# Kernel tuning notes

Measured on AMD Instinct MI355X. Metric: run time of the kernel, lower is better.

## Reference

```python
import jax, jax.numpy as jnp
import numpy as np

B, D, W = 65536, 256, 1024

def setup_inputs() -> dict:
    key = jax.random.key(0)
    k1, k2, k3, k4 = jax.random.split(key, 4)
    z = jax.random.normal(k1, (B, D), dtype=jnp.float32)
    # PyTorch Linear init: U(-1/sqrt(fan_in), 1/sqrt(fan_in))
    s1 = 1.0 / np.sqrt(D)
    s2 = 1.0 / np.sqrt(W)
    W1 = jax.random.uniform(k2, (W, D), dtype=jnp.float32, minval=-s1, maxval=s1)
    b1 = jax.random.uniform(k3, (W,), dtype=jnp.float32, minval=-s1, maxval=s1)
    W2 = jax.random.uniform(k4, (D, W), dtype=jnp.float32, minval=-s2, maxval=s2)
    t = jnp.zeros((1,), dtype=jnp.float32)
    return {"t": t, "z": z, "W1": W1, "b1": b1, "W2": W2}

def reference(t, z, W1, b1, W2):
    # dynamics: f(z) = W2 @ softplus(W1 z + b1)   (t is unused; autonomous ODE)
    pre = z @ W1.T + b1                 # [B, W]
    h = jax.nn.softplus(pre)            # [B, W]
    dz_dt = h @ W2.T                    # [B, D]
    # trace of Jacobian, analytic:
    # df_i/dz_i = sum_j W2[i,j] * sigmoid(pre_j) * W1[j,i]
    # => trace_b = sigmoid(pre_b) . M, with M_j = sum_i W1[j,i] * W2[i,j]
    M = jnp.einsum('ji,ij->j', W1, W2)  # [W]
    trace = jax.nn.sigmoid(pre) @ M     # [B]
    dlogpz_dt = -trace[:, None]         # [B, 1]
    return (dz_dt, dlogpz_dt)
```

## Files before the change

### kernel.cpp

```cpp
#include <hip/hip_runtime.h>
#include <cstdint>
#include <cstddef>

#define B_N 65536
#define D_N 256
#define W_N 1024

typedef __bf16 bf16x8 __attribute__((ext_vector_type(8)));
typedef float f32x4 __attribute__((ext_vector_type(4)));
typedef unsigned short u16x8 __attribute__((ext_vector_type(8)));

__device__ __forceinline__ unsigned short f2bf(float f) {
  unsigned u = __float_as_uint(f);
  u += 0x7fffu + ((u >> 16) & 1u);
  return (unsigned short)(u >> 16);
}

__global__ __launch_bounds__(256) void prep_kernel(
    const float* __restrict__ W1, const float* __restrict__ W2,
    unsigned short* __restrict__ W1b, unsigned short* __restrict__ W2b,
    float* __restrict__ M) {
  const int j = blockIdx.x;
  const int t = threadIdx.x;
  const int gid = j * 256 + t;
  float w1 = W1[gid];
  float w2g = W2[gid];
  W1b[gid] = f2bf(w1);
  W2b[gid] = f2bf(w2g);
  float p = w1 * W2[t * W_N + j];
  #pragma unroll
  for (int m = 32; m; m >>= 1) p += __shfl_xor(p, m);
  __shared__ float red[4];
  if ((t & 63) == 0) red[t >> 6] = p;
  __syncthreads();
  if (t == 0) M[j] = red[0] + red[1] + red[2] + red[3];
}

__global__ __launch_bounds__(256, 2) void flow_kernel(
    const float* __restrict__ z, const float* __restrict__ b1,
    const unsigned short* __restrict__ W1b, const unsigned short* __restrict__ W2b,
    const float* __restrict__ M, float* __restrict__ dz, float* __restrict__ tr) {
  __shared__ __align__(16) unsigned short z_sh[64 * 256];
  __shared__ __align__(16) unsigned short h_sh[64 * 256];

  const int tid = threadIdx.x;
  const int wave = tid >> 6;
  const int lane = tid & 63;
  const int l15 = lane & 15;
  const int q = lane >> 4;
  const int row0 = blockIdx.x * 64;

  #pragma unroll
  for (int it = 0; it < 8; ++it) {
    int id = it * 256 + tid;
    int m = id >> 5;
    int o = id & 31;
    const float* gp = z + (size_t)(row0 + m) * D_N + o * 8;
    f32x4 a = *(const f32x4*)gp;
    f32x4 b = *(const f32x4*)(gp + 4);
    u16x8 v;
    v[0] = f2bf(a[0]); v[1] = f2bf(a[1]); v[2] = f2bf(a[2]); v[3] = f2bf(a[3]);
    v[4] = f2bf(b[0]); v[5] = f2bf(b[1]); v[6] = f2bf(b[2]); v[7] = f2bf(b[3]);
    int slot = (((o >> 2) * 4 + (m >> 4)) * 64 + (o & 3) * 16 + (m & 15));
    *(u16x8*)(z_sh + slot * 8) = v;
  }
  __syncthreads();

  f32x4 acc2[4][4];
  #pragma unroll
  for (int a = 0; a < 4; ++a)
    #pragma unroll
    for (int b = 0; b < 4; ++b)
      acc2[a][b] = (f32x4){0.f, 0.f, 0.f, 0.f};
  float trp[4][4];
  #pragma unroll
  for (int a = 0; a < 4; ++a)
    #pragma unroll
    for (int r = 0; r < 4; ++r) trp[a][r] = 0.f;

  #pragma unroll 1
  for (int c = 0; c < 4; ++c) {
    const int j0 = c * 256;

    f32x4 acc1[4][4];
    #pragma unroll
    for (int a = 0; a < 4; ++a)
      #pragma unroll
      for (int b = 0; b < 4; ++b)
        acc1[a][b] = (f32x4){0.f, 0.f, 0.f, 0.f};

    #pragma unroll
    for (int ks = 0; ks < 8; ++ks) {
      bf16x8 afr[4];
      #pragma unroll
      for (int tm = 0; tm < 4; ++tm)
        afr[tm] = *(const bf16x8*)(z_sh + ((ks * 4 + tm) * 64 + lane) * 8);
      bf16x8 bfr[4];
      #pragma unroll
      for (int tn = 0; tn < 4; ++tn)
        bfr[tn] = *(const bf16x8*)(W1b +
            (size_t)(j0 + wave * 64 + tn * 16 + l15) * D_N + ks * 32 + q * 8);
      #pragma unroll
      for (int tm = 0; tm < 4; ++tm)
        #pragma unroll
        for (int tn = 0; tn < 4; ++tn)
          acc1[tm][tn] = __builtin_amdgcn_mfma_f32_16x16x32_bf16(
              afr[tm], bfr[tn], acc1[tm][tn], 0, 0, 0);
    }

    __syncthreads();

    #pragma unroll
    for (int tn = 0; tn < 4; ++tn) {
      const int jl = wave * 64 + tn * 16 + l15;
      const int jg = j0 + jl;
      const float b1v = b1[jg];
      const float Mv = M[jg];
      const int slot_base = ((jl >> 5) * 4) * 64 + ((jl >> 3) & 3) * 16;
      const int byte_lo = (jl & 7);
      #pragma unroll
      for (int tm = 0; tm < 4; ++tm) {
        #pragma unroll
        for (int r = 0; r < 4; ++r) {
          float x = acc1[tm][tn][r] + b1v;
          float e = __expf(-fabsf(x));
          float inv = __builtin_amdgcn_rcpf(1.0f + e);
          float sig = (x >= 0.f) ? inv : (1.0f - inv);
          float sp = fmaxf(x, 0.f) + __logf(1.0f + e);
          trp[tm][r] += sig * Mv;
          int slot = slot_base + tm * 64 + (q * 4 + r);
          h_sh[slot * 8 + byte_lo] = f2bf(sp);
        }
      }
    }
    __syncthreads();

    #pragma unroll
    for (int ks = 0; ks < 8; ++ks) {
      bf16x8 afr[4];
      #pragma unroll
      for (int tm = 0; tm < 4; ++tm)
        afr[tm] = *(const bf16x8*)(h_sh + ((ks * 4 + tm) * 64 + lane) * 8);
      bf16x8 bfr[4];
      #pragma unroll
      for (int tn = 0; tn < 4; ++tn)
        bfr[tn] = *(const bf16x8*)(W2b +
            (size_t)(wave * 64 + tn * 16 + l15) * W_N + j0 + ks * 32 + q * 8);
      #pragma unroll
      for (int tm = 0; tm < 4; ++tm)
        #pragma unroll
        for (int tn = 0; tn < 4; ++tn)
          acc2[tm][tn] = __builtin_amdgcn_mfma_f32_16x16x32_bf16(
              afr[tm], bfr[tn], acc2[tm][tn], 0, 0, 0);
    }
  }

  #pragma unroll
  for (int tm = 0; tm < 4; ++tm)
    #pragma unroll
    for (int tn = 0; tn < 4; ++tn)
      #pragma unroll
      for (int r = 0; r < 4; ++r)
        dz[(size_t)(row0 + tm * 16 + q * 4 + r) * D_N + wave * 64 + tn * 16 + l15] =
            acc2[tm][tn][r];

  #pragma unroll
  for (int tm = 0; tm < 4; ++tm) {
    #pragma unroll
    for (int r = 0; r < 4; ++r) {
      float v = trp[tm][r];
      v += __shfl_xor(v, 1);
      v += __shfl_xor(v, 2);
      v += __shfl_xor(v, 4);
      v += __shfl_xor(v, 8);
      if (l15 == 0) atomicAdd(tr + row0 + tm * 16 + q * 4 + r, -v);
    }
  }
}

extern "C" void kernel_launch(void* const* d_in, const int* in_sizes, int n_in,
                              void* d_out, int out_size, void* d_ws, size_t ws_size,
                              hipStream_t stream) {
  (void)in_sizes; (void)n_in; (void)out_size; (void)ws_size;
  const float* z  = (const float*)d_in[1];
  const float* W1 = (const float*)d_in[2];
  const float* b1 = (const float*)d_in[3];
  const float* W2 = (const float*)d_in[4];
  float* dz = (float*)d_out;
  float* tr = dz + (size_t)B_N * D_N;

  unsigned short* W1b = (unsigned short*)d_ws;
  unsigned short* W2b = W1b + (size_t)W_N * D_N;
  float* M = (float*)(W2b + (size_t)W_N * D_N);

  hipMemsetAsync(tr, 0, B_N * sizeof(float), stream);
  prep_kernel<<<dim3(W_N), dim3(256), 0, stream>>>(W1, W2, W1b, W2b, M);
  flow_kernel<<<dim3(B_N / 64), dim3(256), 0, stream>>>(z, b1, W1b, W2b, M, dz, tr);
}
```

Before: 261.5 us.

## Software-pipeline GEMM1 of next chunk with softplus epilogue of current chunk

Restructures the chunk loop so the first GEMM for the next 256-column chunk runs interleaved with the transcendental epilogue (softplus/sigmoid) of the current chunk. Two accumulator sets are used, which lets MFMA work overlap with VALU exp/log work. The second GEMM also runs at raised wave priority via s_setprio. The cost is more live registers (two 4x4 f32x4 accumulator sets plus acc2), which risks spilling or lower occupancy under launch_bounds(256,2).

```diff
diff --git a/kernel.cpp b/kernel.cpp
--- a/kernel.cpp
+++ b/kernel.cpp
@@ -78,81 +78,113 @@
     #pragma unroll
     for (int r = 0; r < 4; ++r) trp[a][r] = 0.f;
 
+  f32x4 accA[4][4], accB[4][4];
+
+#define ZERO_ACC(A_)                                                          \
+  _Pragma("unroll") for (int za_ = 0; za_ < 4; ++za_)                         \
+  _Pragma("unroll") for (int zb_ = 0; zb_ < 4; ++zb_)                         \
+    A_[za_][zb_] = (f32x4){0.f, 0.f, 0.f, 0.f};
+
+#define G1_STEP(J0_, ACC_, S_) {                                              \
+  bf16x8 afr_[4];                                                             \
+  _Pragma("unroll") for (int tm_ = 0; tm_ < 4; ++tm_)                         \
+    afr_[tm_] = *(const bf16x8*)(z_sh + (((S_) * 4 + tm_) * 64 + lane) * 8);  \
+  bf16x8 bfr_[4];                                                             \
+  _Pragma("unroll") for (int tn_ = 0; tn_ < 4; ++tn_)                         \
+    bfr_[tn_] = *(const bf16x8*)(W1b +                                        \
+        (size_t)((J0_) + wave * 64 + tn_ * 16 + l15) * D_N + (S_) * 32 + q * 8); \
+  _Pragma("unroll") for (int tm_ = 0; tm_ < 4; ++tm_)                         \
+  _Pragma("unroll") for (int tn_ = 0; tn_ < 4; ++tn_)                         \
+    ACC_[tm_][tn_] = __builtin_amdgcn_mfma_f32_16x16x32_bf16(                 \
+        afr_[tm_], bfr_[tn_], ACC_[tm_][tn_], 0, 0, 0);                       \
+}
+
+#define EPI_PRELOAD(J0_)                                                      \
+  float b1c_[4], Mc_[4];                                                      \
+  _Pragma("unroll") for (int tn_ = 0; tn_ < 4; ++tn_) {                       \
+    int jg_ = (J0_) + wave * 64 + tn_ * 16 + l15;                             \
+    b1c_[tn_] = b1[jg_];                                                      \
+    Mc_[tn_] = M[jg_];                                                        \
+  }
+
+#define EPI_STEP(ACC_, S_) {                                                  \
+  const int etn_ = (S_) >> 1;                                                 \
+  const int jl_ = wave * 64 + etn_ * 16 + l15;                                \
+  const int slot_base_ = ((jl_ >> 5) * 4) * 64 + ((jl_ >> 3) & 3) * 16;       \
+  const int byte_lo_ = jl_ & 7;                                               \
+  const float b1v_ = b1c_[etn_];                                              \
+  const float Mv_ = Mc_[etn_];                                                \
+  _Pragma("unroll") for (int tt_ = 0; tt_ < 2; ++tt_) {                       \
+    const int etm_ = ((S_) & 1) * 2 + tt_;                                    \
+    _Pragma("unroll") for (int r_ = 0; r_ < 4; ++r_) {                        \
+      float x_ = ACC_[etm_][etn_][r_] + b1v_;                                 \
+      float e_ = __expf(-fabsf(x_));                                          \
+      float inv_ = __builtin_amdgcn_rcpf(1.0f + e_);                          \
+      float sig_ = (x_ >= 0.f) ? inv_ : (1.0f - inv_);                        \
+      float sp_ = fmaxf(x_, 0.f) + __logf(1.0f + e_);                         \
+      trp[etm_][r_] += sig_ * Mv_;                                            \
+      int slot_ = slot_base_ + etm_ * 64 + (q * 4 + r_);                      \
+      h_sh[slot_ * 8 + byte_lo_] = f2bf(sp_);                                 \
+    }                                                                         \
+  }                                                                           \
+}
+
+#define MIX_FULL(J0E_, ACCE_, J0G_, ACCG_) {                                  \
+  EPI_PRELOAD(J0E_);                                                          \
+  ZERO_ACC(ACCG_);                                                            \
+  _Pragma("unroll") for (int s_ = 0; s_ < 8; ++s_) {                          \
+    G1_STEP(J0G_, ACCG_, s_);                                                 \
+    EPI_STEP(ACCE_, s_);                                                      \
+  }                                                                           \
+}
+
+#define EPI_ONLY(J0E_, ACCE_) {                                               \
+  EPI_PRELOAD(J0E_);                                                          \
+  _Pragma("unroll") for (int s_ = 0; s_ < 8; ++s_) {                          \
+    EPI_STEP(ACCE_, s_);                                                      \
+  }                                                                           \
+}
+
+#define G2_CHUNK(J0_) {                                                       \
+  __builtin_amdgcn_s_setprio(1);                                              \
+  _Pragma("unroll") for (int ks_ = 0; ks_ < 8; ++ks_) {                       \
+    bf16x8 afr_[4];                                                           \
+    _Pragma("unroll") for (int tm_ = 0; tm_ < 4; ++tm_)                       \
+      afr_[tm_] = *(const bf16x8*)(h_sh + ((ks_ * 4 + tm_) * 64 + lane) * 8); \
+    bf16x8 bfr_[4];                                                           \
+    _Pragma("unroll") for (int tn_ = 0; tn_ < 4; ++tn_)                       \
+      bfr_[tn_] = *(const bf16x8*)(W2b +                                      \
+          (size_t)(wave * 64 + tn_ * 16 + l15) * W_N + (J0_) + ks_ * 32 + q * 8); \
+    _Pragma("unroll") for (int tm_ = 0; tm_ < 4; ++tm_)                       \
+    _Pragma("unroll") for (int tn_ = 0; tn_ < 4; ++tn_)                       \
+      acc2[tm_][tn_] = __builtin_amdgcn_mfma_f32_16x16x32_bf16(               \
+          afr_[tm_], bfr_[tn_], acc2[tm_][tn_], 0, 0, 0);                     \
+  }                                                                           \
+  __builtin_amdgcn_s_setprio(0);                                              \
+}
+
+  ZERO_ACC(accA);
+  #pragma unroll
+  for (int s = 0; s < 8; ++s) { G1_STEP(0, accA, s); }
+
   #pragma unroll 1
-  for (int c = 0; c < 4; ++c) {
-    const int j0 = c * 256;
-
-    f32x4 acc1[4][4];
-    #pragma unroll
-    for (int a = 0; a < 4; ++a)
-      #pragma unroll
-      for (int b = 0; b < 4; ++b)
-        acc1[a][b] = (f32x4){0.f, 0.f, 0.f, 0.f};
-
-    #pragma unroll
-    for (int ks = 0; ks < 8; ++ks) {
-      bf16x8 afr[4];
-      #pragma unroll
-      for (int tm = 0; tm < 4; ++tm)
-        afr[tm] = *(const bf16x8*)(z_sh + ((ks * 4 + tm) * 64 + lane) * 8);
-      bf16x8 bfr[4];
-      #pragma unroll
-      for (int tn = 0; tn < 4; ++tn)
-        bfr[tn] = *(const bf16x8*)(W1b +
-            (size_t)(j0 + wave * 64 + tn * 16 + l15) * D_N + ks * 32 + q * 8);
-      #pragma unroll
-      for (int tm = 0; tm < 4; ++tm)
-        #pragma unroll
-        for (int tn = 0; tn < 4; ++tn)
-          acc1[tm][tn] = __builtin_amdgcn_mfma_f32_16x16x32_bf16(
-              afr[tm], bfr[tn], acc1[tm][tn], 0, 0, 0);
+  for (int cc = 0; cc < 2; ++cc) {
+    const int j0_0 = cc * 512;
+    const int j0_1 = j0_0 + 256;
+
+    MIX_FULL(j0_0, accA, j0_1, accB);
+    __syncthreads();
+    G2_CHUNK(j0_0);
+    __syncthreads();
+
+    if (cc == 0) {
+      MIX_FULL(j0_1, accB, 512, accA);
+    } else {
+      EPI_ONLY(j0_1, accB);
     }
-
-    __syncthreads();
-
-    #pragma unroll
-    for (int tn = 0; tn < 4; ++tn) {
-      const int jl = wave * 64 + tn * 16 + l15;
-      const int jg = j0 + jl;
-      const float b1v = b1[jg];
-      const float Mv = M[jg];
-      const int slot_base = ((jl >> 5) * 4) * 64 + ((jl >> 3) & 3) * 16;
-      const int byte_lo = (jl & 7);
-      #pragma unroll
-      for (int tm = 0; tm < 4; ++tm) {
-        #pragma unroll
-        for (int r = 0; r < 4; ++r) {
-          float x = acc1[tm][tn][r] + b1v;
-          float e = __expf(-fabsf(x));
-          float inv = __builtin_amdgcn_rcpf(1.0f + e);
-          float sig = (x >= 0.f) ? inv : (1.0f - inv);
-          float sp = fmaxf(x, 0.f) + __logf(1.0f + e);
-          trp[tm][r] += sig * Mv;
-          int slot = slot_base + tm * 64 + (q * 4 + r);
-          h_sh[slot * 8 + byte_lo] = f2bf(sp);
-        }
-      }
-    }
-    __syncthreads();
-
-    #pragma unroll
-    for (int ks = 0; ks < 8; ++ks) {
-      bf16x8 afr[4];
-      #pragma unroll
-      for (int tm = 0; tm < 4; ++tm)
-        afr[tm] = *(const bf16x8*)(h_sh + ((ks * 4 + tm) * 64 + lane) * 8);
-      bf16x8 bfr[4];
-      #pragma unroll
-      for (int tn = 0; tn < 4; ++tn)
-        bfr[tn] = *(const bf16x8*)(W2b +
-            (size_t)(wave * 64 + tn * 16 + l15) * W_N + j0 + ks * 32 + q * 8);
-      #pragma unroll
-      for (int tm = 0; tm < 4; ++tm)
-        #pragma unroll
-        for (int tn = 0; tn < 4; ++tn)
-          acc2[tm][tn] = __builtin_amdgcn_mfma_f32_16x16x32_bf16(
-              afr[tm], bfr[tn], acc2[tm][tn], 0, 0, 0);
-    }
+    __syncthreads();
+    G2_CHUNK(j0_1);
+    __syncthreads();
   }
 
   #pragma unroll
```

Result: slower. 308.3 us (+17.9%).

## Prefetch weight fragments three stages ahead and use LDS-only barriers

Applied to the files above, without the earlier changes.

Weight fragments for both GEMMs are now held in a three-deep register ring and prefetched several k-steps ahead, so global loads overlap with MFMA work. The W2 prefetch is issued before the softplus phase so its latency is hidden behind the elementwise work. b1 and M are loaded early, and __syncthreads is replaced by a barrier that waits only on LDS counters, so outstanding global loads are not drained. This adds register pressure (24 extra bf16x8 fragments) under launch_bounds(256,2), which may cause spilling or lower occupancy.

```diff
diff --git a/kernel.cpp b/kernel.cpp
--- a/kernel.cpp
+++ b/kernel.cpp
@@ -14,6 +14,13 @@
   unsigned u = __float_as_uint(f);
   u += 0x7fffu + ((u >> 16) & 1u);
   return (unsigned short)(u >> 16);
+}
+
+__device__ __forceinline__ void lds_barrier() {
+  __builtin_amdgcn_sched_barrier(0);
+  asm volatile("s_waitcnt lgkmcnt(0)" ::: "memory");
+  __builtin_amdgcn_s_barrier();
+  __builtin_amdgcn_sched_barrier(0);
 }
 
 __global__ __launch_bounds__(256) void prep_kernel(
@@ -82,6 +89,26 @@
   for (int c = 0; c < 4; ++c) {
     const int j0 = c * 256;
 
+    const unsigned short* w1p[4];
+    #pragma unroll
+    for (int tn = 0; tn < 4; ++tn)
+      w1p[tn] = W1b + (size_t)(j0 + wave * 64 + tn * 16 + l15) * D_N + q * 8;
+
+    bf16x8 bq[3][4];
+    #pragma unroll
+    for (int p = 0; p < 3; ++p)
+      #pragma unroll
+      for (int tn = 0; tn < 4; ++tn)
+        bq[p][tn] = *(const bf16x8*)(w1p[tn] + p * 32);
+
+    float b1c[4], Mc[4];
+    #pragma unroll
+    for (int tn = 0; tn < 4; ++tn) {
+      int jg = j0 + wave * 64 + tn * 16 + l15;
+      b1c[tn] = b1[jg];
+      Mc[tn] = M[jg];
+    }
+
     f32x4 acc1[4][4];
     #pragma unroll
     for (int a = 0; a < 4; ++a)
@@ -95,27 +122,37 @@
       #pragma unroll
       for (int tm = 0; tm < 4; ++tm)
         afr[tm] = *(const bf16x8*)(z_sh + ((ks * 4 + tm) * 64 + lane) * 8);
-      bf16x8 bfr[4];
+      #pragma unroll
+      for (int tm = 0; tm < 4; ++tm)
+        #pragma unroll
+        for (int tn = 0; tn < 4; ++tn)
+          acc1[tm][tn] = __builtin_amdgcn_mfma_f32_16x16x32_bf16(
+              afr[tm], bq[ks % 3][tn], acc1[tm][tn], 0, 0, 0);
+      if (ks < 5) {
+        #pragma unroll
+        for (int tn = 0; tn < 4; ++tn)
+          bq[ks % 3][tn] = *(const bf16x8*)(w1p[tn] + (ks + 3) * 32);
+      }
+    }
+
+    const unsigned short* w2p[4];
+    #pragma unroll
+    for (int tn = 0; tn < 4; ++tn)
+      w2p[tn] = W2b + (size_t)(wave * 64 + tn * 16 + l15) * W_N + j0 + q * 8;
+    bf16x8 cq[3][4];
+    #pragma unroll
+    for (int p = 0; p < 3; ++p)
       #pragma unroll
       for (int tn = 0; tn < 4; ++tn)
-        bfr[tn] = *(const bf16x8*)(W1b +
-            (size_t)(j0 + wave * 64 + tn * 16 + l15) * D_N + ks * 32 + q * 8);
-      #pragma unroll
-      for (int tm = 0; tm < 4; ++tm)
-        #pragma unroll
-        for (int tn = 0; tn < 4; ++tn)
-          acc1[tm][tn] = __builtin_amdgcn_mfma_f32_16x16x32_bf16(
-              afr[tm], bfr[tn], acc1[tm][tn], 0, 0, 0);
-    }
-
-    __syncthreads();
+        cq[p][tn] = *(const bf16x8*)(w2p[tn] + p * 32);
+
+    lds_barrier();
 
     #pragma unroll
     for (int tn = 0; tn < 4; ++tn) {
       const int jl = wave * 64 + tn * 16 + l15;
-      const int jg = j0 + jl;
-      const float b1v = b1[jg];
-      const float Mv = M[jg];
+      const float b1v = b1c[tn];
+      const float Mv = Mc[tn];
       const int slot_base = ((jl >> 5) * 4) * 64 + ((jl >> 3) & 3) * 16;
       const int byte_lo = (jl & 7);
       #pragma unroll
@@ -133,7 +170,8 @@
         }
       }
     }
-    __syncthreads();
+
+    lds_barrier();
 
     #pragma unroll
     for (int ks = 0; ks < 8; ++ks) {
@@ -141,17 +179,17 @@
       #pragma unroll
       for (int tm = 0; tm < 4; ++tm)
         afr[tm] = *(const bf16x8*)(h_sh + ((ks * 4 + tm) * 64 + lane) * 8);
-      bf16x8 bfr[4];
-      #pragma unroll
-      for (int tn = 0; tn < 4; ++tn)
-        bfr[tn] = *(const bf16x8*)(W2b +
-            (size_t)(wave * 64 + tn * 16 + l15) * W_N + j0 + ks * 32 + q * 8);
       #pragma unroll
       for (int tm = 0; tm < 4; ++tm)
         #pragma unroll
         for (int tn = 0; tn < 4; ++tn)
           acc2[tm][tn] = __builtin_amdgcn_mfma_f32_16x16x32_bf16(
-              afr[tm], bfr[tn], acc2[tm][tn], 0, 0, 0);
+              afr[tm], cq[ks % 3][tn], acc2[tm][tn], 0, 0, 0);
+      if (ks < 5) {
+        #pragma unroll
+        for (int tn = 0; tn < 4; ++tn)
+          cq[ks % 3][tn] = *(const bf16x8*)(w2p[tn] + (ks + 3) * 32);
+      }
     }
   }
 
```

Result: faster. 255.3 us (-2.4%).

## Split hidden chunk into 128-wide halves to cut LDS and raise occupancy

Applied to the files above, without the earlier changes.

Each 256-wide hidden chunk is now handled as two 128-wide sub-chunks, which halves the h_sh buffer and the acc1 register tile. Launch bounds move from 2 to 3 blocks per CU so more waves can hide latency. The __syncthreads calls become a custom LDS barrier that waits only on lgkmcnt, and the b1/M loads are hoisted ahead of the first GEMM. The cost is twice as many barriers per chunk and a tighter register budget, which could cause spills.

```diff
diff --git a/kernel.cpp b/kernel.cpp
--- a/kernel.cpp
+++ b/kernel.cpp
@@ -14,6 +14,13 @@
   unsigned u = __float_as_uint(f);
   u += 0x7fffu + ((u >> 16) & 1u);
   return (unsigned short)(u >> 16);
+}
+
+__device__ __forceinline__ void lds_barrier() {
+  __builtin_amdgcn_sched_barrier(0);
+  asm volatile("s_waitcnt lgkmcnt(0)" ::: "memory");
+  __builtin_amdgcn_s_barrier();
+  __builtin_amdgcn_sched_barrier(0);
 }
 
 __global__ __launch_bounds__(256) void prep_kernel(
@@ -36,15 +43,15 @@
   if (t == 0) M[j] = red[0] + red[1] + red[2] + red[3];
 }
 
-__global__ __launch_bounds__(256, 2) void flow_kernel(
+__global__ __launch_bounds__(256, 3) void flow_kernel(
     const float* __restrict__ z, const float* __restrict__ b1,
     const unsigned short* __restrict__ W1b, const unsigned short* __restrict__ W2b,
     const float* __restrict__ M, float* __restrict__ dz, float* __restrict__ tr) {
   __shared__ __align__(16) unsigned short z_sh[64 * 256];
-  __shared__ __align__(16) unsigned short h_sh[64 * 256];
+  __shared__ __align__(16) unsigned short h_sh[64 * 128];
 
   const int tid = threadIdx.x;
-  const int wave = tid >> 6;
+  const int w = tid >> 6;
   const int lane = tid & 63;
   const int l15 = lane & 15;
   const int q = lane >> 4;
@@ -80,78 +87,88 @@
 
   #pragma unroll 1
   for (int c = 0; c < 4; ++c) {
-    const int j0 = c * 256;
-
-    f32x4 acc1[4][4];
-    #pragma unroll
-    for (int a = 0; a < 4; ++a)
-      #pragma unroll
-      for (int b = 0; b < 4; ++b)
-        acc1[a][b] = (f32x4){0.f, 0.f, 0.f, 0.f};
-
-    #pragma unroll
-    for (int ks = 0; ks < 8; ++ks) {
-      bf16x8 afr[4];
-      #pragma unroll
-      for (int tm = 0; tm < 4; ++tm)
-        afr[tm] = *(const bf16x8*)(z_sh + ((ks * 4 + tm) * 64 + lane) * 8);
-      bf16x8 bfr[4];
-      #pragma unroll
-      for (int tn = 0; tn < 4; ++tn)
-        bfr[tn] = *(const bf16x8*)(W1b +
-            (size_t)(j0 + wave * 64 + tn * 16 + l15) * D_N + ks * 32 + q * 8);
-      #pragma unroll
-      for (int tm = 0; tm < 4; ++tm)
+    #pragma unroll
+    for (int p = 0; p < 2; ++p) {
+      const int jb = c * 256 + p * 128;
+
+      f32x4 acc1[4][2];
+      #pragma unroll
+      for (int a = 0; a < 4; ++a)
+        #pragma unroll
+        for (int b = 0; b < 2; ++b)
+          acc1[a][b] = (f32x4){0.f, 0.f, 0.f, 0.f};
+
+      float b1c[2], Mc[2];
+      #pragma unroll
+      for (int tn = 0; tn < 2; ++tn) {
+        int jg = jb + w * 32 + tn * 16 + l15;
+        b1c[tn] = b1[jg];
+        Mc[tn] = M[jg];
+      }
+
+      #pragma unroll
+      for (int ks = 0; ks < 8; ++ks) {
+        bf16x8 afr[4];
+        #pragma unroll
+        for (int tm = 0; tm < 4; ++tm)
+          afr[tm] = *(const bf16x8*)(z_sh + ((ks * 4 + tm) * 64 + lane) * 8);
+        bf16x8 bfr[2];
+        #pragma unroll
+        for (int tn = 0; tn < 2; ++tn)
+          bfr[tn] = *(const bf16x8*)(W1b +
+              (size_t)(jb + w * 32 + tn * 16 + l15) * D_N + ks * 32 + q * 8);
+        #pragma unroll
+        for (int tm = 0; tm < 4; ++tm)
+          #pragma unroll
+          for (int tn = 0; tn < 2; ++tn)
+            acc1[tm][tn] = __builtin_amdgcn_mfma_f32_16x16x32_bf16(
+                afr[tm], bfr[tn], acc1[tm][tn], 0, 0, 0);
+      }
+
+      lds_barrier();
+
+      #pragma unroll
+      for (int tn = 0; tn < 2; ++tn) {
+        const float b1v = b1c[tn];
+        const float Mv = Mc[tn];
+        const int grp = ((tn * 16 + l15) >> 3) & 3;
+        const int elem = l15 & 7;
+        #pragma unroll
+        for (int tm = 0; tm < 4; ++tm) {
+          #pragma unroll
+          for (int r = 0; r < 4; ++r) {
+            float x = acc1[tm][tn][r] + b1v;
+            float ex = __expf(-fabsf(x));
+            float inv = __builtin_amdgcn_rcpf(1.0f + ex);
+            float sig = (x >= 0.f) ? inv : (1.0f - inv);
+            float sp = fmaxf(x, 0.f) + __logf(1.0f + ex);
+            trp[tm][r] += sig * Mv;
+            int slot = (w * 4 + tm) * 64 + grp * 16 + (q * 4 + r);
+            h_sh[slot * 8 + elem] = f2bf(sp);
+          }
+        }
+      }
+
+      lds_barrier();
+
+      #pragma unroll
+      for (int ks = 0; ks < 4; ++ks) {
+        bf16x8 afr[4];
+        #pragma unroll
+        for (int tm = 0; tm < 4; ++tm)
+          afr[tm] = *(const bf16x8*)(h_sh + ((ks * 4 + tm) * 64 + lane) * 8);
+        bf16x8 bfr[4];
         #pragma unroll
         for (int tn = 0; tn < 4; ++tn)
-          acc1[tm][tn] = __builtin_amdgcn_mfma_f32_16x16x32_bf16(
-              afr[tm], bfr[tn], acc1[tm][tn], 0, 0, 0);
-    }
-
-    __syncthreads();
-
-    #pragma unroll
-    for (int tn = 0; tn < 4; ++tn) {
-      const int jl = wave * 64 + tn * 16 + l15;
-      const int jg = j0 + jl;
-      const float b1v = b1[jg];
-      const float Mv = M[jg];
-      const int slot_base = ((jl >> 5) * 4) * 64 + ((jl >> 3) & 3) * 16;
-      const int byte_lo = (jl & 7);
-      #pragma unroll
-      for (int tm = 0; tm < 4; ++tm) {
-        #pragma unroll
-        for (int r = 0; r < 4; ++r) {
-          float x = acc1[tm][tn][r] + b1v;
-          float e = __expf(-fabsf(x));
-          float inv = __builtin_amdgcn_rcpf(1.0f + e);
-          float sig = (x >= 0.f) ? inv : (1.0f - inv);
-          float sp = fmaxf(x, 0.f) + __logf(1.0f + e);
-          trp[tm][r] += sig * Mv;
-          int slot = slot_base + tm * 64 + (q * 4 + r);
-          h_sh[slot * 8 + byte_lo] = f2bf(sp);
-        }
-      }
-    }
-    __syncthreads();
-
-    #pragma unroll
-    for (int ks = 0; ks < 8; ++ks) {
-      bf16x8 afr[4];
-      #pragma unroll
-      for (int tm = 0; tm < 4; ++tm)
-        afr[tm] = *(const bf16x8*)(h_sh + ((ks * 4 + tm) * 64 + lane) * 8);
-      bf16x8 bfr[4];
-      #pragma unroll
-      for (int tn = 0; tn < 4; ++tn)
-        bfr[tn] = *(const bf16x8*)(W2b +
-            (size_t)(wave * 64 + tn * 16 + l15) * W_N + j0 + ks * 32 + q * 8);
-      #pragma unroll
-      for (int tm = 0; tm < 4; ++tm)
-        #pragma unroll
-        for (int tn = 0; tn < 4; ++tn)
-          acc2[tm][tn] = __builtin_amdgcn_mfma_f32_16x16x32_bf16(
-              afr[tm], bfr[tn], acc2[tm][tn], 0, 0, 0);
+          bfr[tn] = *(const bf16x8*)(W2b +
+              (size_t)(w * 64 + tn * 16 + l15) * W_N + jb + ks * 32 + q * 8);
+        #pragma unroll
+        for (int tm = 0; tm < 4; ++tm)
+          #pragma unroll
+          for (int tn = 0; tn < 4; ++tn)
+            acc2[tm][tn] = __builtin_amdgcn_mfma_f32_16x16x32_bf16(
+                afr[tm], bfr[tn], acc2[tm][tn], 0, 0, 0);
+      }
     }
   }
 
@@ -161,7 +178,7 @@
     for (int tn = 0; tn < 4; ++tn)
       #pragma unroll
       for (int r = 0; r < 4; ++r)
-        dz[(size_t)(row0 + tm * 16 + q * 4 + r) * D_N + wave * 64 + tn * 16 + l15] =
+        dz[(size_t)(row0 + tm * 16 + q * 4 + r) * D_N + w * 64 + tn * 16 + l15] =
             acc2[tm][tn][r];
 
   #pragma unroll
```

Result: slower. 281.2 us (+7.6%).
